# Kernel optimization log

Measured on AMD Instinct MI355X. Metric: run time of the kernel, lower is better.

Reference implementation:

```python
import jax, jax.numpy as jnp
import numpy as np

N, I, D, K = 64, 8192, 128, 16


def setup_inputs() -> dict:
    key = jax.random.key(0)
    k1, k2 = jax.random.split(key)
    x = jax.random.normal(k1, (N, I, D), dtype=jnp.float32)
    # each point belongs to one of k clusters of its own batch element -> offset n*K
    ci = jax.random.randint(k2, (N, I), 0, K) + jnp.arange(N)[:, None] * K
    return {
        "feature_matrix_batch": x,
        "cluster_index": ci.reshape(-1).astype(jnp.int32),  # [N*I]
        "k": K,
    }


def reference(feature_matrix_batch, cluster_index, k):
    n, i, d = feature_matrix_batch.shape
    flat = feature_matrix_batch.reshape(-1, d)  # [N*I, D]
    # scatter_max over segment ids -> [N*k, D]
    out = jax.ops.segment_max(flat, cluster_index, num_segments=n * k)
    return out.reshape(n, k, d)
```

## Files before the change

### kernel.cpp

```cpp
#include <hip/hip_runtime.h>
#include <stdint.h>

#define NB 64
#define NI 8192
#define ND 128
#define NK 16
#define SEG (NK * ND)
#define OUT_ELEMS (NB * SEG)
#define MAPPED_NEG_INF 0x007FFFFFu

#define PPB_A 1024
#define BPB_A (NI / PPB_A)
#define GRID_A (NB * BPB_A)
#define WS_NEEDED ((size_t)GRID_A * SEG * 4)

typedef float f4 __attribute__((ext_vector_type(4)));
typedef uint32_t u4 __attribute__((ext_vector_type(4)));

__device__ __forceinline__ uint32_t map_f32(float f) {
    uint32_t b = __float_as_uint(f);
    return b ^ ((uint32_t)((int32_t)b >> 31) | 0x80000000u);
}
__device__ __forceinline__ uint32_t unmap_u32(uint32_t m) {
    return (m & 0x80000000u) ? (m ^ 0x80000000u) : ~m;
}

__global__ __launch_bounds__(1024, 8) void seg_partial(
        const float* __restrict__ x,
        const int* __restrict__ ci,
        uint32_t* __restrict__ ws) {
    __shared__ uint32_t loc[SEG];
    __shared__ int cidx[PPB_A];

    const int t = threadIdx.x;
    const int b = blockIdx.x;
    const int batch = b >> 3;
    const int row0 = batch * NI + (b & (BPB_A - 1)) * PPB_A;

    for (int i = t; i < SEG; i += 1024) loc[i] = MAPPED_NEG_INF;
    if (t < PPB_A / 4) {
        int4 c = ((const int4*)(ci + row0))[t];
        const int base = batch * NK;
        c.x -= base; c.y -= base; c.z -= base; c.w -= base;
        ((int4*)cidx)[t] = c;
    }
    __syncthreads();

    const int lane32 = t & 31;
    const int rsub = t >> 5;
    const f4* xrow = (const f4*)(x + (size_t)row0 * ND) + lane32;

    #pragma unroll 2
    for (int it = 0; it < PPB_A / 32; ++it) {
        const int i = it * 32 + rsub;
        const int c = cidx[i];
        f4 v = xrow[(size_t)i * (ND / 4)];
        uint32_t* lp = &loc[(c << 7) + lane32];
        atomicMax(&lp[0],  map_f32(v.x));
        atomicMax(&lp[32], map_f32(v.y));
        atomicMax(&lp[64], map_f32(v.z));
        atomicMax(&lp[96], map_f32(v.w));
    }
    __syncthreads();

    if (t < SEG / 4) {
        const int c = t >> 5;
        const int dq = t & 31;
        u4 r;
        r.x = loc[(c << 7) + dq];
        r.y = loc[(c << 7) + 32 + dq];
        r.z = loc[(c << 7) + 64 + dq];
        r.w = loc[(c << 7) + 96 + dq];
        ((u4*)(ws + (size_t)b * SEG))[t] = r;
    }
}

__global__ __launch_bounds__(256) void seg_reduce(
        const uint32_t* __restrict__ ws,
        uint32_t* __restrict__ out) {
    const int idx = blockIdx.x * 256 + threadIdx.x;
    const int batch = idx >> 9;
    const int o4 = idx & (SEG / 4 - 1);
    const u4* p = (const u4*)(ws + (size_t)batch * BPB_A * SEG) + o4;
    u4 m;
    m.x = m.y = m.z = m.w = MAPPED_NEG_INF;
    #pragma unroll
    for (int j = 0; j < BPB_A; ++j) {
        u4 v = p[(size_t)j * (SEG / 4)];
        m.x = v.x > m.x ? v.x : m.x;
        m.y = v.y > m.y ? v.y : m.y;
        m.z = v.z > m.z ? v.z : m.z;
        m.w = v.w > m.w ? v.w : m.w;
    }
    u4 r;
    r.x = unmap_u32(m.x); r.y = unmap_u32(m.y);
    r.z = unmap_u32(m.z); r.w = unmap_u32(m.w);
    ((u4*)out)[idx] = r;
}

#define PPB_B 256
#define BPB_B (NI / PPB_B)

__global__ __launch_bounds__(256) void seg_init(uint32_t* __restrict__ out) {
    int idx = blockIdx.x * 256 + threadIdx.x;
    out[idx] = MAPPED_NEG_INF;
}

__global__ __launch_bounds__(256, 8) void seg_max_kernel(
        const float* __restrict__ x,
        const int* __restrict__ ci,
        uint32_t* __restrict__ out) {
    __shared__ uint32_t loc[SEG];
    __shared__ int cidx[PPB_B];

    const int t = threadIdx.x;
    const int b = blockIdx.x;
    const int batch = b >> 5;
    const int row0 = batch * NI + (b & (BPB_B - 1)) * PPB_B;

    for (int i = t; i < SEG; i += 256) loc[i] = MAPPED_NEG_INF;
    cidx[t] = ci[row0 + t] - batch * NK;
    __syncthreads();

    const int lane32 = t & 31;
    const int rsub = t >> 5;
    const f4* xrow = (const f4*)(x + (size_t)row0 * ND) + lane32;

    for (int it = 0; it < PPB_B / 8; ++it) {
        const int i = it * 8 + rsub;
        const int c = cidx[i];
        f4 v = xrow[(size_t)i * (ND / 4)];
        uint32_t* lp = &loc[(c << 7) + lane32];
        atomicMax(&lp[0],  map_f32(v.x));
        atomicMax(&lp[32], map_f32(v.y));
        atomicMax(&lp[64], map_f32(v.z));
        atomicMax(&lp[96], map_f32(v.w));
    }
    __syncthreads();

    uint32_t* ob = out + (size_t)batch * SEG;
    for (int o = t; o < SEG; o += 256) {
        const int c = o >> 7;
        const int d = o & 127;
        uint32_t v = loc[(c << 7) + ((d & 3) << 5) + (d >> 2)];
        if (v != MAPPED_NEG_INF) atomicMax(&ob[o], v);
    }
}

__global__ __launch_bounds__(256) void seg_decode(uint32_t* __restrict__ out) {
    int idx = blockIdx.x * 256 + threadIdx.x;
    out[idx] = unmap_u32(out[idx]);
}

extern "C" void kernel_launch(void* const* d_in, const int* in_sizes, int n_in,
                              void* d_out, int out_size, void* d_ws, size_t ws_size,
                              hipStream_t stream) {
    const float* x = (const float*)d_in[0];
    const int* ci = (const int*)d_in[1];
    uint32_t* out = (uint32_t*)d_out;

    if (ws_size >= WS_NEEDED) {
        uint32_t* ws = (uint32_t*)d_ws;
        seg_partial<<<GRID_A, 1024, 0, stream>>>(x, ci, ws);
        seg_reduce<<<OUT_ELEMS / 4 / 256, 256, 0, stream>>>(ws, out);
    } else {
        seg_init<<<OUT_ELEMS / 256, 256, 0, stream>>>(out);
        seg_max_kernel<<<NB * BPB_B, 256, 0, stream>>>(x, ci, out);
        seg_decode<<<OUT_ELEMS / 256, 256, 0, stream>>>(out);
    }
}
```

Before: 47.55 us.

## Fuse partial and reduce kernels via last-block-done counter per batch

Merges the partial segment-max kernel and the separate reduction kernel into one launch. Each block increments a per-batch atomic counter after writing its partial, and the last block of each batch reduces the eight partials and writes the decoded output. This removes a kernel launch and the gap between the two kernels, but adds a memset launch for the counters, fences, and a serial tail where a few last blocks do the reduction.

Result: slower. 77.72 us (+63.4%).

```diff
diff --git a/kernel.cpp b/kernel.cpp
--- a/kernel.cpp
+++ b/kernel.cpp
@@ -12,7 +12,8 @@
 #define PPB_A 1024
 #define BPB_A (NI / PPB_A)
 #define GRID_A (NB * BPB_A)
-#define WS_NEEDED ((size_t)GRID_A * SEG * 4)
+#define CNT_OFF ((size_t)GRID_A * SEG)
+#define WS_NEEDED (((size_t)GRID_A * SEG + NB) * 4)
 
 typedef float f4 __attribute__((ext_vector_type(4)));
 typedef uint32_t u4 __attribute__((ext_vector_type(4)));
@@ -25,12 +26,14 @@
     return (m & 0x80000000u) ? (m ^ 0x80000000u) : ~m;
 }
 
-__global__ __launch_bounds__(1024, 8) void seg_partial(
+__global__ __launch_bounds__(1024, 8) void seg_fused(
         const float* __restrict__ x,
         const int* __restrict__ ci,
-        uint32_t* __restrict__ ws) {
+        uint32_t* __restrict__ ws,
+        uint32_t* __restrict__ out) {
     __shared__ uint32_t loc[SEG];
     __shared__ int cidx[PPB_A];
+    __shared__ int sIsLast;
 
     const int t = threadIdx.x;
     const int b = blockIdx.x;
@@ -73,29 +76,33 @@
         r.w = loc[(c << 7) + 96 + dq];
         ((u4*)(ws + (size_t)b * SEG))[t] = r;
     }
-}
+    __syncthreads();
 
-__global__ __launch_bounds__(256) void seg_reduce(
-        const uint32_t* __restrict__ ws,
-        uint32_t* __restrict__ out) {
-    const int idx = blockIdx.x * 256 + threadIdx.x;
-    const int batch = idx >> 9;
-    const int o4 = idx & (SEG / 4 - 1);
-    const u4* p = (const u4*)(ws + (size_t)batch * BPB_A * SEG) + o4;
-    u4 m;
-    m.x = m.y = m.z = m.w = MAPPED_NEG_INF;
-    #pragma unroll
-    for (int j = 0; j < BPB_A; ++j) {
-        u4 v = p[(size_t)j * (SEG / 4)];
-        m.x = v.x > m.x ? v.x : m.x;
-        m.y = v.y > m.y ? v.y : m.y;
-        m.z = v.z > m.z ? v.z : m.z;
-        m.w = v.w > m.w ? v.w : m.w;
+    if (t == 0) {
+        __threadfence();
+        unsigned old = atomicAdd(ws + CNT_OFF + batch, 1u);
+        sIsLast = (old == BPB_A - 1);
+        if (sIsLast) __threadfence();
     }
-    u4 r;
-    r.x = unmap_u32(m.x); r.y = unmap_u32(m.y);
-    r.z = unmap_u32(m.z); r.w = unmap_u32(m.w);
-    ((u4*)out)[idx] = r;
+    __syncthreads();
+
+    if (sIsLast && t < SEG / 4) {
+        const u4* p = (const u4*)(ws + (size_t)batch * BPB_A * SEG) + t;
+        u4 m;
+        m.x = m.y = m.z = m.w = MAPPED_NEG_INF;
+        #pragma unroll
+        for (int j = 0; j < BPB_A; ++j) {
+            u4 v = p[(size_t)j * (SEG / 4)];
+            m.x = v.x > m.x ? v.x : m.x;
+            m.y = v.y > m.y ? v.y : m.y;
+            m.z = v.z > m.z ? v.z : m.z;
+            m.w = v.w > m.w ? v.w : m.w;
+        }
+        u4 r;
+        r.x = unmap_u32(m.x); r.y = unmap_u32(m.y);
+        r.z = unmap_u32(m.z); r.w = unmap_u32(m.w);
+        ((u4*)(out + (size_t)batch * SEG))[t] = r;
+    }
 }
 
 #define PPB_B 256
@@ -161,8 +168,8 @@
 
     if (ws_size >= WS_NEEDED) {
         uint32_t* ws = (uint32_t*)d_ws;
-        seg_partial<<<GRID_A, 1024, 0, stream>>>(x, ci, ws);
-        seg_reduce<<<OUT_ELEMS / 4 / 256, 256, 0, stream>>>(ws, out);
+        hipMemsetAsync((char*)d_ws + CNT_OFF * 4, 0, NB * 4, stream);
+        seg_fused<<<GRID_A, 1024, 0, stream>>>(x, ci, ws, out);
     } else {
         seg_init<<<OUT_ELEMS / 256, 256, 0, stream>>>(out);
         seg_max_kernel<<<NB * BPB_B, 256, 0, stream>>>(x, ci, out);
```
